# Optimization experiments

Measured on AMD Instinct MI355X. Metric: run time of the kernel, lower is better.

## Reference

```python
import jax, jax.numpy as jnp
import numpy as np

LOSS_WEIGHT = 0.01  # balancing_loss_alpha


def setup_inputs() -> dict:
    key = jax.random.key(0)
    L, T, E = 32, 16384, 64  # num_layers, tokens, n_routed_experts
    router_logits = jax.random.normal(key, (L, T, E), dtype=jnp.float32)
    return {
        "router_logits": router_logits,
        "n_routed_experts": E,
        "num_experts_per_tok": 8,
    }


def reference(router_logits, n_routed_experts, num_experts_per_tok):
    # loss_type == 'softmax', global_average single-device path
    L, T, E = router_logits.shape
    logits = router_logits.astype(jnp.float32)
    routing_weights = jax.nn.softmax(logits, axis=-1)  # [L, T, E]
    # top-k expert selection per token
    _, selected = jax.lax.top_k(routing_weights, num_experts_per_tok)  # [L, T, K]
    # per-layer histogram of expert assignments (== offset + histc in torch)
    counts = jax.vmap(lambda s: jnp.bincount(s.reshape(-1), length=n_routed_experts))(
        selected
    )  # [L, E] int
    tokens_per_expert = counts.astype(routing_weights.dtype)
    scale = n_routed_experts / (T * num_experts_per_tok)
    rw_mean = routing_weights.mean(axis=1)  # [L, E]
    loss = (scale * (tokens_per_expert * rw_mean).sum(-1)).sum()
    return loss * LOSS_WEIGHT
```

## Files before the change

kernel.cpp:

```cpp
#include <hip/hip_runtime.h>
#include <float.h>

#define NL 32
#define NT 16384
#define NE 64
#define NK 8
#define LOG2E 1.4426950408889634f

#define DPP_QUAD_XOR1 0xB1
#define DPP_QUAD_XOR2 0x4E
#define DPP_ROW_ROR4  0x124
#define DPP_ROW_ROR8  0x128

template <int CTRL>
__device__ __forceinline__ float dppmv(float v) {
    return __int_as_float(
        __builtin_amdgcn_update_dpp(0, __float_as_int(v), CTRL, 0xF, 0xF, true));
}

__device__ __forceinline__ float grp_max(float v) {
    v = fmaxf(v, dppmv<DPP_QUAD_XOR1>(v));
    v = fmaxf(v, dppmv<DPP_QUAD_XOR2>(v));
    v = fmaxf(v, dppmv<DPP_ROW_ROR4>(v));
    v = fmaxf(v, dppmv<DPP_ROW_ROR8>(v));
    return v;
}
__device__ __forceinline__ float grp_sum(float v) {
    v = v + dppmv<DPP_QUAD_XOR1>(v);
    v = v + dppmv<DPP_QUAD_XOR2>(v);
    v = v + dppmv<DPP_ROW_ROR4>(v);
    v = v + dppmv<DPP_ROW_ROR8>(v);
    return v;
}

__device__ __forceinline__ void ce(float& a, float& b) {
    float hi = fmaxf(a, b);
    float lo = fminf(a, b);
    a = hi; b = lo;
}

__global__ __launch_bounds__(256, 4) void bl_main(const float* __restrict__ logits,
                                                  float* __restrict__ g_w,
                                                  float* __restrict__ g_c) {
    const int tid  = threadIdx.x;
    const int lane = tid & 63;
    const int wv   = tid >> 6;
    const long slab = ((long)blockIdx.x * 4 + wv) * 64;
    const int layer = (int)(slab >> 14);

    const float4* p = (const float4*)(logits + slab * NE);
    float4 v[16];
#pragma unroll
    for (int j = 0; j < 16; ++j) v[j] = p[j * 64 + lane];

    float wacc[4] = {0.f, 0.f, 0.f, 0.f};
    float cacc[4] = {0.f, 0.f, 0.f, 0.f};

#pragma unroll
    for (int j = 0; j < 16; ++j) {
        const float l0 = v[j].x, l1 = v[j].y, l2 = v[j].z, l3 = v[j].w;

        float q0 = l0, q1 = l1, q2 = l2, q3 = l3;
        ce(q0, q1); ce(q2, q3); ce(q0, q2); ce(q1, q3); ce(q1, q2);

        float thr = -FLT_MAX;
#pragma unroll
        for (int k = 0; k < NK; ++k) {
            const float m = grp_max(q0);
            thr = m;
            if (k < NK - 1) {
                const bool hit = (q0 == m);
                q0 = hit ? q1 : q0;
                q1 = hit ? q2 : q1;
                q2 = hit ? q3 : q2;
                q3 = hit ? -FLT_MAX : q3;
            }
        }

        cacc[0] += (l0 >= thr) ? 1.f : 0.f;
        cacc[1] += (l1 >= thr) ? 1.f : 0.f;
        cacc[2] += (l2 >= thr) ? 1.f : 0.f;
        cacc[3] += (l3 >= thr) ? 1.f : 0.f;

        const float x0 = __builtin_amdgcn_exp2f(l0 * LOG2E);
        const float x1 = __builtin_amdgcn_exp2f(l1 * LOG2E);
        const float x2 = __builtin_amdgcn_exp2f(l2 * LOG2E);
        const float x3 = __builtin_amdgcn_exp2f(l3 * LOG2E);
        const float den = grp_sum((x0 + x1) + (x2 + x3));
        const float inv = __builtin_amdgcn_rcpf(den);
        wacc[0] = fmaf(x0, inv, wacc[0]);
        wacc[1] = fmaf(x1, inv, wacc[1]);
        wacc[2] = fmaf(x2, inv, wacc[2]);
        wacc[3] = fmaf(x3, inv, wacc[3]);
    }

#pragma unroll
    for (int r = 0; r < 4; ++r) {
        wacc[r] += __shfl_xor(wacc[r], 16);
        wacc[r] += __shfl_xor(wacc[r], 32);
        cacc[r] += __shfl_xor(cacc[r], 16);
        cacc[r] += __shfl_xor(cacc[r], 32);
    }

    __shared__ float comb[2][NE][4];
    if (lane < 16) {
#pragma unroll
        for (int r = 0; r < 4; ++r) {
            comb[0][lane * 4 + r][wv] = wacc[r];
            comb[1][lane * 4 + r][wv] = cacc[r];
        }
    }
    __syncthreads();
    if (tid < 128) {
        const int s = tid >> 6, e = tid & 63;
        const float val = comb[s][e][0] + comb[s][e][1] + comb[s][e][2] + comb[s][e][3];
        float* dst = s ? g_c : g_w;
        atomicAdd(&dst[layer * NE + e], val);
    }
}

__global__ void bl_final(const float* __restrict__ g_w,
                         const float* __restrict__ g_c,
                         float* __restrict__ out) {
    __shared__ float red[256];
    float p = 0.f;
    for (int i = threadIdx.x; i < NL * NE; i += 256) p += g_c[i] * g_w[i];
    red[threadIdx.x] = p;
    __syncthreads();
    for (int s = 128; s > 0; s >>= 1) {
        if (threadIdx.x < s) red[threadIdx.x] += red[threadIdx.x + s];
        __syncthreads();
    }
    if (threadIdx.x == 0) {
        const float factor = (float)(0.01 * ((double)NE / ((double)NT * NK)) / (double)NT);
        out[0] = red[0] * factor;
    }
}

extern "C" void kernel_launch(void* const* d_in, const int* in_sizes, int n_in,
                              void* d_out, int out_size, void* d_ws, size_t ws_size,
                              hipStream_t stream) {
    const float* logits = (const float*)d_in[0];
    float* g_w = (float*)d_ws;
    float* g_c = g_w + NL * NE;

    hipMemsetAsync(d_ws, 0, 2 * NL * NE * sizeof(float), stream);
    bl_main<<<dim3(2048), dim3(256), 0, stream>>>(logits, g_w, g_c);
    bl_final<<<dim3(1), dim3(256), 0, stream>>>(g_w, g_c, (float*)d_out);
}
```

Measured before the change: 52.97 us.

## Double-buffer logit loads, raise occupancy, and run top-k on exponentials

Replaces the upfront load of all 16 float4 rows per lane with a two-slot rolling buffer that prefetches two rows ahead, and raises the launch-bounds occupancy hint from 4 to 8 blocks. Register pressure drops so more waves can hide memory latency, but each wave now keeps only two loads in flight instead of sixteen. The top-k selection is also done on the exponentials instead of the raw logits, so the exp values computed for the softmax are reused, and the sentinels change to 0 and -1. Ranking on exp is equivalent, but exp2 underflow or ties could change counts in edge cases.

```diff
diff --git a/kernel.cpp b/kernel.cpp
--- a/kernel.cpp
+++ b/kernel.cpp
@@ -39,7 +39,7 @@
     a = hi; b = lo;
 }
 
-__global__ __launch_bounds__(256, 4) void bl_main(const float* __restrict__ logits,
+__global__ __launch_bounds__(256, 8) void bl_main(const float* __restrict__ logits,
                                                   float* __restrict__ g_w,
                                                   float* __restrict__ g_c) {
     const int tid  = threadIdx.x;
@@ -49,21 +49,31 @@
     const int layer = (int)(slab >> 14);
 
     const float4* p = (const float4*)(logits + slab * NE);
-    float4 v[16];
-#pragma unroll
-    for (int j = 0; j < 16; ++j) v[j] = p[j * 64 + lane];
 
     float wacc[4] = {0.f, 0.f, 0.f, 0.f};
     float cacc[4] = {0.f, 0.f, 0.f, 0.f};
 
+    float4 buf[2];
+    buf[0] = p[0 * 64 + lane];
+    buf[1] = p[1 * 64 + lane];
+
 #pragma unroll
     for (int j = 0; j < 16; ++j) {
-        const float l0 = v[j].x, l1 = v[j].y, l2 = v[j].z, l3 = v[j].w;
+        const float4 cur = buf[j & 1];
+        if (j + 2 < 16) buf[j & 1] = p[(j + 2) * 64 + lane];
 
-        float q0 = l0, q1 = l1, q2 = l2, q3 = l3;
+        const float x0 = __builtin_amdgcn_exp2f(cur.x * LOG2E);
+        const float x1 = __builtin_amdgcn_exp2f(cur.y * LOG2E);
+        const float x2 = __builtin_amdgcn_exp2f(cur.z * LOG2E);
+        const float x3 = __builtin_amdgcn_exp2f(cur.w * LOG2E);
+
+        const float den = grp_sum((x0 + x1) + (x2 + x3));
+        const float inv = __builtin_amdgcn_rcpf(den);
+
+        float q0 = x0, q1 = x1, q2 = x2, q3 = x3;
         ce(q0, q1); ce(q2, q3); ce(q0, q2); ce(q1, q3); ce(q1, q2);
 
-        float thr = -FLT_MAX;
+        float thr = 0.f;
 #pragma unroll
         for (int k = 0; k < NK; ++k) {
             const float m = grp_max(q0);
@@ -73,21 +83,15 @@
                 q0 = hit ? q1 : q0;
                 q1 = hit ? q2 : q1;
                 q2 = hit ? q3 : q2;
-                q3 = hit ? -FLT_MAX : q3;
+                q3 = hit ? -1.0f : q3;
             }
         }
 
-        cacc[0] += (l0 >= thr) ? 1.f : 0.f;
-        cacc[1] += (l1 >= thr) ? 1.f : 0.f;
-        cacc[2] += (l2 >= thr) ? 1.f : 0.f;
-        cacc[3] += (l3 >= thr) ? 1.f : 0.f;
+        cacc[0] += (x0 >= thr) ? 1.f : 0.f;
+        cacc[1] += (x1 >= thr) ? 1.f : 0.f;
+        cacc[2] += (x2 >= thr) ? 1.f : 0.f;
+        cacc[3] += (x3 >= thr) ? 1.f : 0.f;
 
-        const float x0 = __builtin_amdgcn_exp2f(l0 * LOG2E);
-        const float x1 = __builtin_amdgcn_exp2f(l1 * LOG2E);
-        const float x2 = __builtin_amdgcn_exp2f(l2 * LOG2E);
-        const float x3 = __builtin_amdgcn_exp2f(l3 * LOG2E);
-        const float den = grp_sum((x0 + x1) + (x2 + x3));
-        const float inv = __builtin_amdgcn_rcpf(den);
         wacc[0] = fmaf(x0, inv, wacc[0]);
         wacc[1] = fmaf(x1, inv, wacc[1]);
         wacc[2] = fmaf(x2, inv, wacc[2]);
```

Result: no change. 52.76 us (-0.4%).
